# Optimization experiments

Hardware: AMD Instinct MI355X
Metric: run time of the kernel (lower is better)

## Reference

```python
import jax, jax.numpy as jnp
import numpy as np

NEG_INF = -jnp.inf


def setup_inputs() -> dict:
    B, V = 128, 128000
    key = jax.random.key(0)
    k1, k2, k3, k4, k5 = jax.random.split(key, 5)
    logits = jax.random.normal(k1, (B, V), dtype=jnp.float32)
    # temperatures in [0.1, 1.0) to avoid divide-by-tiny blowups
    temperatures = jax.random.uniform(k2, (B,), dtype=jnp.float32) * 0.9 + 0.1
    # min_p typically small, in [0, 0.1)
    min_ps = jax.random.uniform(k3, (B,), dtype=jnp.float32) * 0.1
    # top_p in [0.1, 1.0)
    top_ps = jax.random.uniform(k4, (B,), dtype=jnp.float32) * 0.9 + 0.1
    # top_k in [1, 1000)
    top_ks = jax.random.randint(k5, (B,), 1, 1000, dtype=jnp.int32)
    return {"logits": logits, "temperatures": temperatures, "min_ps": min_ps,
            "top_ps": top_ps, "top_ks": top_ks}


def _apply_top_k_top_p(logits, top_ps, top_ks):
    B, V = logits.shape
    sort_idx = jnp.argsort(logits, axis=-1)  # ascending, matches torch sort(descending=False)
    logits_sort = jnp.take_along_axis(logits, sort_idx, axis=-1)
    # top-k: threshold is the (V-k)-th smallest value; mask anything strictly below it
    thresh_idx = (V - top_ks.astype(jnp.int32))[:, None]          # [B,1]
    thresh = jnp.take_along_axis(logits_sort, thresh_idx, axis=-1)  # [B,1]
    logits_sort = jnp.where(logits_sort < thresh, NEG_INF, logits_sort)
    # top-p: drop smallest tokens whose cumulative prob <= 1 - p; never drop the max token
    probs_sort = jax.nn.softmax(logits_sort, axis=-1)
    probs_sum = jnp.cumsum(probs_sort, axis=-1)
    top_p_mask = probs_sum <= (1.0 - top_ps)[:, None]
    top_p_mask = top_p_mask.at[:, -1].set(False)
    logits_sort = jnp.where(top_p_mask, NEG_INF, logits_sort)
    # scatter back to original vocab order
    rows = jnp.arange(B)[:, None]
    return jnp.zeros_like(logits_sort).at[rows, sort_idx].set(logits_sort)


def _apply_min_p(logits, min_ps):
    probs = jax.nn.softmax(logits, axis=-1)
    top_probs = jnp.max(probs, axis=-1, keepdims=True)
    remove = probs < min_ps[:, None] * top_probs
    return jnp.where(remove, NEG_INF, logits)


def reference(logits, temperatures, min_ps, top_ps, top_ks):
    logits = logits.astype(jnp.float32) / temperatures[:, None]
    logits = _apply_top_k_top_p(logits, top_ps, top_ks)
    logits = _apply_min_p(logits, min_ps)
    # torch.multinomial(softmax(logits), 1) == categorical sampling from logits
    sample_key = jax.random.key(42)
    next_tokens = jax.random.categorical(sample_key, logits, axis=-1)  # [B]
    return next_tokens
```

## Files before the change

kernel.cpp:

```cpp
#include <hip/hip_runtime.h>
#include <stdint.h>

#define HBINS 4096
#define CAND 2048
#define NSLICES 16
#define HTHREADS 256
#define CTHREADS 256
#define STHREADS 1024

typedef unsigned int u32;
typedef unsigned long long u64;

__device__ __forceinline__ u32 f2s(float f) {
  u32 b = __float_as_uint(f);
  return b ^ ((b & 0x80000000u) ? 0xFFFFFFFFu : 0x80000000u);
}
__device__ __forceinline__ float s2f(u32 s) {
  u32 b = (s & 0x80000000u) ? (s ^ 0x80000000u) : ~s;
  return __uint_as_float(b);
}
__device__ __forceinline__ u32 rotl32(u32 x, int r) { return (x << r) | (x >> (32 - r)); }

__device__ __forceinline__ u32 threefry_bits(u32 ctr) {
  const u32 ks0 = 0u, ks1 = 42u, ks2 = 0x1BD11BDAu ^ 0u ^ 42u;
  u32 x0 = ks0;
  u32 x1 = ctr + ks1;
#define TFR(r) { x0 += x1; x1 = rotl32(x1, (r)); x1 ^= x0; }
  TFR(13) TFR(15) TFR(26) TFR(6)   x0 += ks1; x1 += ks2 + 1u;
  TFR(17) TFR(29) TFR(16) TFR(24)  x0 += ks2; x1 += ks0 + 2u;
  TFR(13) TFR(15) TFR(26) TFR(6)   x0 += ks0; x1 += ks1 + 3u;
  TFR(17) TFR(29) TFR(16) TFR(24)  x0 += ks1; x1 += ks2 + 4u;
  TFR(13) TFR(15) TFR(26) TFR(6)   x0 += ks2; x1 += ks0 + 5u;
#undef TFR
  return x0 ^ x1;
}

__global__ __launch_bounds__(1024)
void zero_kernel(u32* __restrict__ p, int n) {
  int i = blockIdx.x * 1024 + threadIdx.x;
  if (i < n) p[i] = 0u;
}

__global__ __launch_bounds__(HTHREADS)
void hist_kernel(const float* __restrict__ logits, u32* __restrict__ ghist,
                 int V, int slice_len) {
  const int row = blockIdx.x / NSLICES;
  const int sl  = blockIdx.x % NSLICES;
  const int tid = threadIdx.x;
  __shared__ u32 h[HBINS];
  for (int i = tid; i < HBINS; i += HTHREADS) h[i] = 0u;
  __syncthreads();
  int rem = V - sl * slice_len;
  if (rem > slice_len) rem = slice_len;
  if (rem < 0) rem = 0;
  const float* src = logits + (size_t)row * (size_t)V + (size_t)sl * slice_len;
  const int n4 = rem >> 2;
  const float4* p4 = (const float4*)src;
  for (int i = tid; i < n4; i += HTHREADS) {
    float4 w = p4[i];
    atomicAdd(&h[f2s(w.x) >> 20], 1u);
    atomicAdd(&h[f2s(w.y) >> 20], 1u);
    atomicAdd(&h[f2s(w.z) >> 20], 1u);
    atomicAdd(&h[f2s(w.w) >> 20], 1u);
  }
  for (int i = (n4 << 2) + tid; i < rem; i += HTHREADS)
    atomicAdd(&h[f2s(src[i]) >> 20], 1u);
  __syncthreads();
  u32* gh = ghist + (size_t)row * HBINS;
  for (int i = tid; i < HBINS; i += HTHREADS) {
    u32 c = h[i];
    if (c) atomicAdd(&gh[i], c);
  }
}

__global__ __launch_bounds__(CTHREADS)
void collect_kernel(const float* __restrict__ logits,
                    const float* __restrict__ temps,
                    const int* __restrict__ topks,
                    const u32* __restrict__ ghist,
                    u32* __restrict__ gcount, u32* __restrict__ gcs,
                    u64* __restrict__ gcand, int V, int slice_len) {
  const int row = blockIdx.x / NSLICES;
  const int sl  = blockIdx.x % NSLICES;
  const int tid = threadIdx.x;

  __shared__ u32 hist[HBINS];
  __shared__ u64 stage[CAND];
  __shared__ u32 part[CTHREADS];
  __shared__ u32 chunk[64];
  __shared__ int sh_cnt, sh_thr, sh_base;

  const u32* gh = ghist + (size_t)row * HBINS;
  for (int i = tid; i < HBINS; i += CTHREADS) hist[i] = gh[i];
  __syncthreads();

  {
    u32 s = 0;
    for (int j = 0; j < 16; ++j) s += hist[tid * 16 + j];
    part[tid] = s;
  }
  __syncthreads();
  if (tid < 64) {
    u32 s = part[tid * 4] + part[tid * 4 + 1] + part[tid * 4 + 2] + part[tid * 4 + 3];
    chunk[tid] = s;
  }
  __syncthreads();
  if (tid == 0) {
    int k = topks[row];
    if (k < 1) k = 1;
    if (k > V) k = V;
    const u32 ku = (u32)k;
    u32 acc = 0;
    int cstar = 0;
    for (int c = 63; c >= 0; --c) {
      if (acc + chunk[c] >= ku) { cstar = c; break; }
      acc += chunk[c];
    }
    int pstar = cstar * 4;
    for (int p = cstar * 4 + 3; p >= cstar * 4; --p) {
      if (acc + part[p] >= ku) { pstar = p; break; }
      acc += part[p];
    }
    int bstar = pstar * 16;
    for (int bq = pstar * 16 + 15; bq >= pstar * 16; --bq) {
      acc += hist[bq];
      if (acc >= ku) { bstar = bq; break; }
    }
    sh_thr = bstar;
    sh_cnt = 0;
    if (sl == 0) gcs[row] = (acc < (u32)CAND ? acc : (u32)CAND);
  }
  __syncthreads();

  const u32 thr = ((u32)sh_thr) << 20;
  const float t = temps[row];
  int rem = V - sl * slice_len;
  if (rem > slice_len) rem = slice_len;
  if (rem < 0) rem = 0;
  const float* src = logits + (size_t)row * (size_t)V + (size_t)sl * slice_len;
  const u32 ibase = (u32)(sl * slice_len);
  const int n4 = rem >> 2;
  const float4* p4 = (const float4*)src;
  for (int i = tid; i < n4; i += CTHREADS) {
    float4 w = p4[i];
    u32 sx = f2s(w.x), sy = f2s(w.y), sz = f2s(w.z), sw = f2s(w.w);
    if (sx >= thr) { int pos = atomicAdd(&sh_cnt, 1); if (pos < CAND) stage[pos] = ((u64)f2s(w.x / t) << 32) | (ibase + 4u * i + 0u); }
    if (sy >= thr) { int pos = atomicAdd(&sh_cnt, 1); if (pos < CAND) stage[pos] = ((u64)f2s(w.y / t) << 32) | (ibase + 4u * i + 1u); }
    if (sz >= thr) { int pos = atomicAdd(&sh_cnt, 1); if (pos < CAND) stage[pos] = ((u64)f2s(w.z / t) << 32) | (ibase + 4u * i + 2u); }
    if (sw >= thr) { int pos = atomicAdd(&sh_cnt, 1); if (pos < CAND) stage[pos] = ((u64)f2s(w.w / t) << 32) | (ibase + 4u * i + 3u); }
  }
  for (int i = (n4 << 2) + tid; i < rem; i += CTHREADS) {
    float l = src[i];
    if (f2s(l) >= thr) { int pos = atomicAdd(&sh_cnt, 1); if (pos < CAND) stage[pos] = ((u64)f2s(l / t) << 32) | (ibase + (u32)i); }
  }
  __syncthreads();
  int n = sh_cnt;
  if (n > CAND) n = CAND;
  if (tid == 0) sh_base = (int)atomicAdd(&gcount[row], (u32)n);
  __syncthreads();
  const int base = sh_base;
  u64* gc = gcand + (size_t)row * CAND;
  for (int i = tid; i < n; i += CTHREADS) {
    int dst = base + i;
    if (dst < CAND) gc[dst] = stage[i];
  }
}

__global__ __launch_bounds__(STHREADS)
void Sampler_73529840107542_kernel(const float* __restrict__ minps,
                                   const float* __restrict__ topps,
                                   const int* __restrict__ topks,
                                   const u32* __restrict__ gcs,
                                   const u64* __restrict__ gcand,
                                   int* __restrict__ out, int V) {
  const int b = blockIdx.x;
  const int tid = threadIdx.x;
  const float one_minus_p = 1.0f - topps[b];
  const float minp = minps[b];
  int k = topks[b];
  if (k < 1) k = 1;
  if (k > V) k = V;

  __shared__ __align__(16) unsigned char arena[34816];
  u64* cand   = (u64*)(arena);
  float* bufA = (float*)(arena + 16384);
  float* bufB = (float*)(arena + 24576);
  unsigned char* keepf = arena + 32768;
  u64* red64  = (u64*)(arena + 16384);
  float* redA = (float*)(arena + 16384);
  float* redB = (float*)(arena + 24576);

  __shared__ int sh_lb;
  __shared__ u32 sh_Ts;
  __shared__ float sh_m, sh_Z1, sh_Z2;

  const int cs = (int)gcs[b];
  int SN = 64;
  while (SN < cs) SN <<= 1;

  const u64* gc = gcand + (size_t)b * CAND;
  for (int c = tid; c < SN; c += STHREADS)
    cand[c] = (c < cs) ? gc[c] : 0xFFFFFFFFFFFFFFFFull;
  __syncthreads();

  for (int size = 2; size <= SN; size <<= 1) {
    for (int stride = size >> 1; stride > 0; stride >>= 1) {
      for (int i = tid; i < SN; i += STHREADS) {
        int j = i ^ stride;
        if (j > i) {
          u64 a = cand[i], bb = cand[j];
          bool asc = ((i & size) == 0);
          if ((a > bb) == asc) { cand[i] = bb; cand[j] = a; }
        }
      }
      __syncthreads();
    }
  }

  if (tid == 0) {
    int ti = cs - k; if (ti < 0) ti = 0;
    sh_Ts = (u32)(cand[ti] >> 32);
    sh_m  = s2f((u32)(cand[cs - 1] >> 32));
  }
  __syncthreads();
  const u32 Ts = sh_Ts;
  const float m = sh_m;

  for (int c = tid; c < cs; c += STHREADS) {
    u32 s = (u32)(cand[c] >> 32);
    if (s >= Ts && (c == 0 || (u32)(cand[c - 1] >> 32) < Ts)) sh_lb = c;
  }
  __syncthreads();
  const int lb = sh_lb;

  for (int c = tid; c < CAND; c += STHREADS) {
    float e = 0.0f;
    if (c < cs) {
      u32 s = (u32)(cand[c] >> 32);
      if (s >= Ts) e = expf(s2f(s) - m);
    }
    bufA[c] = e;
  }
  __syncthreads();

  {
    float local = bufA[tid] + bufA[tid + STHREADS];
    redB[tid] = local;
    __syncthreads();
    for (int s = STHREADS >> 1; s > 0; s >>= 1) {
      if (tid < s) redB[tid] += redB[tid + s];
      __syncthreads();
    }
    if (tid == 0) sh_Z1 = redB[0];
    __syncthreads();
  }

  const float Z1 = sh_Z1;
  for (int c = tid; c < CAND; c += STHREADS) bufA[c] = bufA[c] / Z1;
  __syncthreads();
  if (tid == 0) {
    float acc = 0.0f;
    for (int c = lb; c < cs; ++c) {
      acc += bufA[c];
      bufB[c] = acc;
    }
  }
  __syncthreads();

  for (int c = tid; c < CAND; c += STHREADS) {
    unsigned char kf = 0;
    if (c < cs) {
      u32 s = (u32)(cand[c] >> 32);
      if (s >= Ts && (c == cs - 1 || bufB[c] > one_minus_p)) kf = 1;
    }
    keepf[c] = kf;
  }
  __syncthreads();

  {
    float local = 0.0f;
    for (int c = tid; c < CAND; c += STHREADS) {
      if (keepf[c]) {
        u32 s = (u32)(cand[c] >> 32);
        local += expf(s2f(s) - m);
      }
    }
    redA[tid] = local;
    __syncthreads();
    for (int s = STHREADS >> 1; s > 0; s >>= 1) {
      if (tid < s) redA[tid] += redA[tid + s];
      __syncthreads();
    }
    if (tid == 0) sh_Z2 = redA[0];
    __syncthreads();
  }

  {
    const float Z2 = sh_Z2;
    const float rhs = minp * (1.0f / Z2);
    for (int c = tid; c < CAND; c += STHREADS) {
      if (keepf[c]) {
        u32 s = (u32)(cand[c] >> 32);
        float p2 = expf(s2f(s) - m) / Z2;
        if (p2 < rhs) keepf[c] = 0;
      }
    }
  }
  __syncthreads();

  {
    const float TINY = 1.17549435082228750797e-38f;
    u64 best = 0ull;
    for (int c = lb + tid; c < cs; c += STHREADS) {
      if (!keepf[c]) continue;
      u32 s = (u32)(cand[c] >> 32);
      u32 idx = (u32)(cand[c] & 0xFFFFFFFFull);
      float x = s2f(s);
      u32 bits = threefry_bits((u32)b * (u32)V + idx);
      float f = __uint_as_float((bits >> 9) | 0x3f800000u) - 1.0f;
      float u = fmaxf(TINY, f * 1.0f + TINY);
      float g = -logf(-logf(u));
      float sc = g + x;
      u64 key = ((u64)f2s(sc) << 32) | (u64)(0xFFFFFFFFu - idx);
      if (key > best) best = key;
    }
    red64[tid] = best;
    __syncthreads();
    for (int s = STHREADS >> 1; s > 0; s >>= 1) {
      if (tid < s) { u64 o = red64[tid + s]; if (o > red64[tid]) red64[tid] = o; }
      __syncthreads();
    }
    if (tid == 0) out[b] = (int)(0xFFFFFFFFu - (u32)(red64[0] & 0xFFFFFFFFull));
  }
}

extern "C" void kernel_launch(void* const* d_in, const int* in_sizes, int n_in,
                              void* d_out, int out_size, void* d_ws, size_t ws_size,
                              hipStream_t stream) {
  const float* logits = (const float*)d_in[0];
  const float* temps  = (const float*)d_in[1];
  const float* minps  = (const float*)d_in[2];
  const float* topps  = (const float*)d_in[3];
  const int*   topks  = (const int*)d_in[4];
  const int B = in_sizes[1];
  const int V = in_sizes[0] / B;
  (void)n_in; (void)out_size; (void)ws_size;

  u32* ghist  = (u32*)d_ws;
  u32* gcount = ghist + (size_t)B * HBINS;
  u32* gcs    = gcount + B;
  u64* gcand  = (u64*)(gcs + B);

  const int nz = B * HBINS + 2 * B;
  const int slice_len = (((V + NSLICES - 1) / NSLICES) + 3) & ~3;

  zero_kernel<<<dim3((nz + 1023) / 1024), dim3(1024), 0, stream>>>(ghist, nz);
  hist_kernel<<<dim3(B * NSLICES), dim3(HTHREADS), 0, stream>>>(logits, ghist, V, slice_len);
  collect_kernel<<<dim3(B * NSLICES), dim3(CTHREADS), 0, stream>>>(
      logits, temps, topks, ghist, gcount, gcs, gcand, V, slice_len);
  Sampler_73529840107542_kernel<<<dim3(B), dim3(STHREADS), 0, stream>>>(
      minps, topps, topks, gcs, gcand, (int*)d_out, V);
}
```

Baseline: 202.1 us.

## Split threshold selection into own kernel and use register/shuffle bitonic sort and scan

```diff
diff --git a/kernel.cpp b/kernel.cpp
--- a/kernel.cpp
+++ b/kernel.cpp
@@ -20,6 +20,12 @@
   return __uint_as_float(b);
 }
 __device__ __forceinline__ u32 rotl32(u32 x, int r) { return (x << r) | (x >> (32 - r)); }
+
+__device__ __forceinline__ u64 shfl_xor_u64(u64 v, int mask) {
+  int lo = __shfl_xor((int)(u32)v, mask, 64);
+  int hi = __shfl_xor((int)(u32)(v >> 32), mask, 64);
+  return ((u64)(u32)hi << 32) | (u32)lo;
+}
 
 __device__ __forceinline__ u32 threefry_bits(u32 ctr) {
   const u32 ks0 = 0u, ks1 = 42u, ks2 = 0x1BD11BDAu ^ 0u ^ 42u;
@@ -73,27 +79,18 @@
   }
 }
 
-__global__ __launch_bounds__(CTHREADS)
-void collect_kernel(const float* __restrict__ logits,
-                    const float* __restrict__ temps,
-                    const int* __restrict__ topks,
-                    const u32* __restrict__ ghist,
-                    u32* __restrict__ gcount, u32* __restrict__ gcs,
-                    u64* __restrict__ gcand, int V, int slice_len) {
-  const int row = blockIdx.x / NSLICES;
-  const int sl  = blockIdx.x % NSLICES;
+__global__ __launch_bounds__(256)
+void select_kernel(const u32* __restrict__ ghist, const int* __restrict__ topks,
+                   u32* __restrict__ gthr, u32* __restrict__ gcs,
+                   u32* __restrict__ gcount, int V) {
+  const int row = blockIdx.x;
   const int tid = threadIdx.x;
-
   __shared__ u32 hist[HBINS];
-  __shared__ u64 stage[CAND];
-  __shared__ u32 part[CTHREADS];
+  __shared__ u32 part[256];
   __shared__ u32 chunk[64];
-  __shared__ int sh_cnt, sh_thr, sh_base;
-
   const u32* gh = ghist + (size_t)row * HBINS;
-  for (int i = tid; i < HBINS; i += CTHREADS) hist[i] = gh[i];
-  __syncthreads();
-
+  for (int i = tid; i < HBINS; i += 256) hist[i] = gh[i];
+  __syncthreads();
   {
     u32 s = 0;
     for (int j = 0; j < 16; ++j) s += hist[tid * 16 + j];
@@ -101,8 +98,7 @@
   }
   __syncthreads();
   if (tid < 64) {
-    u32 s = part[tid * 4] + part[tid * 4 + 1] + part[tid * 4 + 2] + part[tid * 4 + 3];
-    chunk[tid] = s;
+    chunk[tid] = part[tid * 4] + part[tid * 4 + 1] + part[tid * 4 + 2] + part[tid * 4 + 3];
   }
   __syncthreads();
   if (tid == 0) {
@@ -126,13 +122,28 @@
       acc += hist[bq];
       if (acc >= ku) { bstar = bq; break; }
     }
-    sh_thr = bstar;
-    sh_cnt = 0;
-    if (sl == 0) gcs[row] = (acc < (u32)CAND ? acc : (u32)CAND);
-  }
-  __syncthreads();
-
-  const u32 thr = ((u32)sh_thr) << 20;
+    gthr[row] = (u32)bstar << 20;
+    gcs[row] = (acc < (u32)CAND ? acc : (u32)CAND);
+    gcount[row] = 0u;
+  }
+}
+
+__global__ __launch_bounds__(CTHREADS)
+void collect_kernel(const float* __restrict__ logits,
+                    const float* __restrict__ temps,
+                    const u32* __restrict__ gthr,
+                    u32* __restrict__ gcount,
+                    u64* __restrict__ gcand, int V, int slice_len) {
+  const int row = blockIdx.x / NSLICES;
+  const int sl  = blockIdx.x % NSLICES;
+  const int tid = threadIdx.x;
+
+  __shared__ u64 stage[CAND];
+  __shared__ int sh_cnt, sh_base;
+  if (tid == 0) sh_cnt = 0;
+  __syncthreads();
+
+  const u32 thr = gthr[row];
   const float t = temps[row];
   int rem = V - sl * slice_len;
   if (rem > slice_len) rem = slice_len;
@@ -143,11 +154,10 @@
   const float4* p4 = (const float4*)src;
   for (int i = tid; i < n4; i += CTHREADS) {
     float4 w = p4[i];
-    u32 sx = f2s(w.x), sy = f2s(w.y), sz = f2s(w.z), sw = f2s(w.w);
-    if (sx >= thr) { int pos = atomicAdd(&sh_cnt, 1); if (pos < CAND) stage[pos] = ((u64)f2s(w.x / t) << 32) | (ibase + 4u * i + 0u); }
-    if (sy >= thr) { int pos = atomicAdd(&sh_cnt, 1); if (pos < CAND) stage[pos] = ((u64)f2s(w.y / t) << 32) | (ibase + 4u * i + 1u); }
-    if (sz >= thr) { int pos = atomicAdd(&sh_cnt, 1); if (pos < CAND) stage[pos] = ((u64)f2s(w.z / t) << 32) | (ibase + 4u * i + 2u); }
-    if (sw >= thr) { int pos = atomicAdd(&sh_cnt, 1); if (pos < CAND) stage[pos] = ((u64)f2s(w.w / t) << 32) | (ibase + 4u * i + 3u); }
+    if (f2s(w.x) >= thr) { int pos = atomicAdd(&sh_cnt, 1); if (pos < CAND) stage[pos] = ((u64)f2s(w.x / t) << 32) | (ibase + 4u * i + 0u); }
+    if (f2s(w.y) >= thr) { int pos = atomicAdd(&sh_cnt, 1); if (pos < CAND) stage[pos] = ((u64)f2s(w.y / t) << 32) | (ibase + 4u * i + 1u); }
+    if (f2s(w.z) >= thr) { int pos = atomicAdd(&sh_cnt, 1); if (pos < CAND) stage[pos] = ((u64)f2s(w.z / t) << 32) | (ibase + 4u * i + 2u); }
+    if (f2s(w.w) >= thr) { int pos = atomicAdd(&sh_cnt, 1); if (pos < CAND) stage[pos] = ((u64)f2s(w.w / t) << 32) | (ibase + 4u * i + 3u); }
   }
   for (int i = (n4 << 2) + tid; i < rem; i += CTHREADS) {
     float l = src[i];
@@ -175,6 +185,8 @@
                                    int* __restrict__ out, int V) {
   const int b = blockIdx.x;
   const int tid = threadIdx.x;
+  const int w = tid >> 6;
+  const int l = tid & 63;
   const float one_minus_p = 1.0f - topps[b];
   const float minp = minps[b];
   int k = topks[b];
@@ -195,27 +207,47 @@
   __shared__ float sh_m, sh_Z1, sh_Z2;
 
   const int cs = (int)gcs[b];
-  int SN = 64;
-  while (SN < cs) SN <<= 1;
-
   const u64* gc = gcand + (size_t)b * CAND;
-  for (int c = tid; c < SN; c += STHREADS)
-    cand[c] = (c < cs) ? gc[c] : 0xFFFFFFFFFFFFFFFFull;
-  __syncthreads();
-
-  for (int size = 2; size <= SN; size <<= 1) {
-    for (int stride = size >> 1; stride > 0; stride >>= 1) {
-      for (int i = tid; i < SN; i += STHREADS) {
-        int j = i ^ stride;
-        if (j > i) {
-          u64 a = cand[i], bb = cand[j];
-          bool asc = ((i & size) == 0);
-          if ((a > bb) == asc) { cand[i] = bb; cand[j] = a; }
+  const int e_lo = (w << 7) + l;
+  const int e_hi = e_lo + 64;
+  const u64 SENT = 0xFFFFFFFFFFFFFFFFull;
+  u64 k0 = (e_lo < cs) ? gc[e_lo] : SENT;
+  u64 k1 = (e_hi < cs) ? gc[e_hi] : SENT;
+
+  for (int size = 2; size <= CAND; size <<= 1) {
+    for (int s = size >> 1; s > 0; s >>= 1) {
+      if (s >= 128) {
+        cand[e_lo] = k0; cand[e_hi] = k1;
+        __syncthreads();
+        u64 p0 = cand[e_lo ^ s], p1 = cand[e_hi ^ s];
+        {
+          bool keepmin = (((e_lo & s) == 0) == ((e_lo & size) == 0));
+          if (keepmin ? (p0 < k0) : (p0 > k0)) k0 = p0;
+        }
+        {
+          bool keepmin = (((e_hi & s) == 0) == ((e_hi & size) == 0));
+          if (keepmin ? (p1 < k1) : (p1 > k1)) k1 = p1;
+        }
+        __syncthreads();
+      } else if (s == 64) {
+        bool asc = ((e_lo & size) == 0);
+        if ((k0 > k1) == asc) { u64 t = k0; k0 = k1; k1 = t; }
+      } else {
+        u64 p0 = shfl_xor_u64(k0, s);
+        u64 p1 = shfl_xor_u64(k1, s);
+        {
+          bool keepmin = (((l & s) == 0) == ((e_lo & size) == 0));
+          if (keepmin ? (p0 < k0) : (p0 > k0)) k0 = p0;
+        }
+        {
+          bool keepmin = (((l & s) == 0) == ((e_hi & size) == 0));
+          if (keepmin ? (p1 < k1) : (p1 > k1)) k1 = p1;
         }
       }
-      __syncthreads();
-    }
-  }
+    }
+  }
+  cand[e_lo] = k0; cand[e_hi] = k1;
+  __syncthreads();
 
   if (tid == 0) {
     int ti = cs - k; if (ti < 0) ti = 0;
@@ -258,11 +290,19 @@
   const float Z1 = sh_Z1;
   for (int c = tid; c < CAND; c += STHREADS) bufA[c] = bufA[c] / Z1;
   __syncthreads();
-  if (tid == 0) {
-    float acc = 0.0f;
-    for (int c = lb; c < cs; ++c) {
-      acc += bufA[c];
-      bufB[c] = acc;
+
+  if (w == 0) {
+    float carry = 0.0f;
+    for (int base = lb; base < cs; base += 64) {
+      int c = base + l;
+      float v = (c < cs) ? bufA[c] : 0.0f;
+      float acc = carry;
+      for (int j = 0; j < 64; ++j) {
+        float t = __shfl(v, j, 64);
+        acc += (l >= j) ? t : 0.0f;
+      }
+      if (c < cs) bufB[c] = acc;
+      carry = __shfl(acc, 63, 64);
     }
   }
   __syncthreads();
@@ -349,15 +389,17 @@
   u32* ghist  = (u32*)d_ws;
   u32* gcount = ghist + (size_t)B * HBINS;
   u32* gcs    = gcount + B;
-  u64* gcand  = (u64*)(gcs + B);
-
-  const int nz = B * HBINS + 2 * B;
+  u32* gthr   = gcs + B;
+  u64* gcand  = (u64*)(gthr + B);
+
+  const int nz = B * HBINS;
   const int slice_len = (((V + NSLICES - 1) / NSLICES) + 3) & ~3;
 
   zero_kernel<<<dim3((nz + 1023) / 1024), dim3(1024), 0, stream>>>(ghist, nz);
   hist_kernel<<<dim3(B * NSLICES), dim3(HTHREADS), 0, stream>>>(logits, ghist, V, slice_len);
+  select_kernel<<<dim3(B), dim3(256), 0, stream>>>(ghist, topks, gthr, gcs, gcount, V);
   collect_kernel<<<dim3(B * NSLICES), dim3(CTHREADS), 0, stream>>>(
-      logits, temps, topks, ghist, gcount, gcs, gcand, V, slice_len);
+      logits, temps, gthr, gcount, gcand, V, slice_len);
   Sampler_73529840107542_kernel<<<dim3(B), dim3(STHREADS), 0, stream>>>(
       minps, topps, topks, gcs, gcand, (int*)d_out, V);
 }
```

New measurement: 170.5 us. -15.6%, faster.
